# Kernel tuning notes

Measured on AMD Instinct MI355X. Metric: run time of the kernel, lower is better.

The kernel has to match this reference:

```python
import jax, jax.numpy as jnp
import numpy as np

N_BATCH = 8192   # rows/cols of score matrix
N_NEG = 16       # negatives per row (init kwarg n)
VOCAB = 100000   # item id range for sel_out


def setup_inputs() -> dict:
    key = jax.random.key(0)
    k1, k2 = jax.random.split(key)
    x = jax.random.normal(k1, (N_BATCH, N_BATCH), dtype=jnp.float32)
    sel_out = jax.random.randint(k2, (N_BATCH,), 0, VOCAB, dtype=jnp.int32)
    return {"x": x, "sel_out": sel_out}


def reference(x, sel_out):
    # mask[i, j] = 1 where item j differs from row i's target item
    mask = (sel_out[None, :] != sel_out[:, None]).astype(x.dtype)  # (n, n)
    # positive term: diagonal holds each row's target score
    pos = -jnp.mean(jax.nn.log_sigmoid(jnp.diagonal(x)))
    # top-N_NEG highest masked scores per row -> negative sample indices
    _, idx = jax.lax.top_k(x * mask, N_NEG)          # idx: (n, N_NEG)
    neg_vals = jnp.take_along_axis(x, idx, axis=1)   # gather raw scores
    # log(1 - sigmoid(v)) == log_sigmoid(-v) (numerically stable form)
    neg = -jnp.mean(jax.nn.log_sigmoid(-neg_vals))
    return pos + neg
```

## Files before the change

### kernel.cpp

```cpp
#include <hip/hip_runtime.h>
#include <math.h>

#define N_ROWS 8192
#define N_NEG 16
#define NBLK (N_ROWS / 8)

__device__ __forceinline__ float log_sigmoid(float v) {
    return fminf(v, 0.0f) - log1pf(__expf(-fabsf(v)));
}

#define INSERT(mv)                                                          \
    {                                                                       \
        unsigned long long ball = __ballot((mv) > tau);                     \
        while (ball) {                                                      \
            const int src = __ffsll((unsigned long long)ball) - 1;          \
            const float cand = __shfl((mv), src);                           \
            ball &= ball - 1;                                               \
            if (cand > tau) {                                               \
                float tprev = __shfl_up(t, 1);                              \
                if (lane == 0) tprev = 3.0e38f;                             \
                t = (t >= cand) ? t : (tprev >= cand ? cand : tprev);       \
                tau = __shfl(t, 15);                                        \
                ball &= __ballot((mv) > tau);         \
            }                                                               \
        }                                                                   \
    }

__global__ __launch_bounds__(512) void nsl_topk_kernel(
        const float* __restrict__ x,
        const int*   __restrict__ sel,
        float*       __restrict__ ws) {
    __shared__ int   sel_lds[N_ROWS];
    __shared__ float partial[8];

    {
        const int4* s4 = reinterpret_cast<const int4*>(sel);
        int4*       d4 = reinterpret_cast<int4*>(sel_lds);
#pragma unroll
        for (int k = 0; k < 4; ++k)
            d4[k * 512 + threadIdx.x] = s4[k * 512 + threadIdx.x];
    }
    __syncthreads();

    const int lane = threadIdx.x & 63;
    const int wid  = threadIdx.x >> 6;
    const int row  = (blockIdx.x << 3) + wid;

    const int    seli = sel_lds[row];
    const float* xrow = x + (size_t)row * N_ROWS;
    const float* pw   = xrow + lane * 4;

    float t   = -3.0e38f;
    float tau = -3.0e38f;

    float4 buf[4];
#pragma unroll
    for (int j = 0; j < 4; ++j)
        buf[j] = *reinterpret_cast<const float4*>(pw + j * 256);

#define BODY(c, PREFETCH)                                                   \
    {                                                                       \
        const float4 v = buf[(c) & 3];                                      \
        if (PREFETCH)                                                       \
            buf[(c) & 3] =                                                  \
                *reinterpret_cast<const float4*>(pw + ((c) + 4) * 256);     \
        const float mxv = fmaxf(fmaxf(v.x, v.y), fmaxf(v.z, v.w));          \
                       \
        if (__any(mxv > tau)) {                                             \
            const int4 s = *reinterpret_cast<const int4*>(                  \
                &sel_lds[((c) << 8) + (lane << 2)]);                        \
            const float m0 = (s.x != seli) ? v.x : 0.0f;                    \
            const float m1 = (s.y != seli) ? v.y : 0.0f;                    \
            const float m2 = (s.z != seli) ? v.z : 0.0f;                    \
            const float m3 = (s.w != seli) ? v.w : 0.0f;                    \
            INSERT(m0);                                                     \
            INSERT(m1);                                                     \
            INSERT(m2);                                                     \
            INSERT(m3);                                                     \
        }                                                                   \
    }

#pragma unroll 1
    for (int g = 0; g < 7; ++g) {
#pragma unroll
        for (int j = 0; j < 4; ++j) BODY((g << 2) + j, true);
    }
#pragma unroll
    for (int j = 0; j < 4; ++j) BODY(28 + j, false);
#undef BODY

    float ls = (lane < 16) ? log_sigmoid(-t) : 0.0f;
    ls += __shfl_xor(ls, 8);
    ls += __shfl_xor(ls, 4);
    ls += __shfl_xor(ls, 2);
    ls += __shfl_xor(ls, 1);

    if (lane == 0) {
        const float d = xrow[row];
        partial[wid] = -log_sigmoid(d) * (1.0f / (float)N_ROWS)
                       - ls * (1.0f / ((float)N_ROWS * (float)N_NEG));
    }
    __syncthreads();

    if (threadIdx.x == 0) {
        float s = 0.0f;
#pragma unroll
        for (int w = 0; w < 8; ++w) s += partial[w];
        ws[blockIdx.x] = s;
    }
}

__global__ __launch_bounds__(256) void nsl_reduce_kernel(
        const float* __restrict__ ws, float* __restrict__ out) {
    __shared__ float red[4];
    float s = 0.0f;
#pragma unroll
    for (int k = 0; k < NBLK / 256; ++k) s += ws[k * 256 + threadIdx.x];
    s += __shfl_xor(s, 32);
    s += __shfl_xor(s, 16);
    s += __shfl_xor(s, 8);
    s += __shfl_xor(s, 4);
    s += __shfl_xor(s, 2);
    s += __shfl_xor(s, 1);
    const int lane = threadIdx.x & 63, wid = threadIdx.x >> 6;
    if (lane == 0) red[wid] = s;
    __syncthreads();
    if (threadIdx.x == 0)
        out[0] = red[0] + red[1] + red[2] + red[3];
}

extern "C" void kernel_launch(void* const* d_in, const int* in_sizes, int n_in,
                              void* d_out, int out_size, void* d_ws, size_t ws_size,
                              hipStream_t stream) {
    const float* x   = (const float*)d_in[0];
    const int*   sel = (const int*)d_in[1];
    float* out = (float*)d_out;
    float* ws  = (float*)d_ws;

    nsl_topk_kernel<<<dim3(NBLK), dim3(512), 0, stream>>>(x, sel, ws);
    nsl_reduce_kernel<<<dim3(1), dim3(256), 0, stream>>>(ws, out);
}
```

Before: 65.04 us.

## Replace wave-serial top-k insertion with per-lane top-5 med3 networks plus exact fallback

Each lane now keeps its own sorted top-5 list, updated branch-free with fmax/fmed3 for every element. The 16 global maxima are then extracted by repeated wave-wide max reductions. If any lane's 5th value still exceeds the 16th global maximum, the lane may have dropped candidates, so the row is rescanned with the old serial ballot/shuffle insertion to stay exact. This removes the per-candidate ballot/shuffle serialization from the common path. In exchange every element costs about five ALU ops, and rows that hit the fallback are read a second time.

```diff
diff --git a/kernel.cpp b/kernel.cpp
--- a/kernel.cpp
+++ b/kernel.cpp
@@ -4,29 +4,34 @@
 #define N_ROWS 8192
 #define N_NEG 16
 #define NBLK (N_ROWS / 8)
+#define NEG_INF (-3.0e38f)
 
 __device__ __forceinline__ float log_sigmoid(float v) {
     return fminf(v, 0.0f) - log1pf(__expf(-fabsf(v)));
 }
 
-#define INSERT(mv)                                                          \
-    {                                                                       \
-        unsigned long long ball = __ballot((mv) > tau);                     \
-        while (ball) {                                                      \
-            const int src = __ffsll((unsigned long long)ball) - 1;          \
-            const float cand = __shfl((mv), src);                           \
-            ball &= ball - 1;                                               \
-            if (cand > tau) {                                               \
-                float tprev = __shfl_up(t, 1);                              \
-                if (lane == 0) tprev = 3.0e38f;                             \
-                t = (t >= cand) ? t : (tprev >= cand ? cand : tprev);       \
-                tau = __shfl(t, 15);                                        \
-                ball &= __ballot((mv) > tau);         \
-            }                                                               \
-        }                                                                   \
+__device__ __forceinline__ float wave_max64(float v) {
+    v = fmaxf(v, __shfl_xor(v, 1));
+    v = fmaxf(v, __shfl_xor(v, 2));
+    v = fmaxf(v, __shfl_xor(v, 4));
+    v = fmaxf(v, __shfl_xor(v, 8));
+    v = fmaxf(v, __shfl_xor(v, 16));
+    v = fmaxf(v, __shfl_xor(v, 32));
+    return v;
+}
+
+#define INS5(cexpr)                                                     \
+    {                                                                   \
+        const float _c = (cexpr);                                       \
+        const float n0 = fmaxf(t0, _c);                                 \
+        const float n1 = __builtin_amdgcn_fmed3f(_c, t0, t1);           \
+        const float n2 = __builtin_amdgcn_fmed3f(_c, t1, t2);           \
+        const float n3 = __builtin_amdgcn_fmed3f(_c, t2, t3);           \
+        const float n4 = __builtin_amdgcn_fmed3f(_c, t3, t4);           \
+        t0 = n0; t1 = n1; t2 = n2; t3 = n3; t4 = n4;                    \
     }
 
-__global__ __launch_bounds__(512) void nsl_topk_kernel(
+__global__ __launch_bounds__(512, 8) void nsl_topk_kernel(
         const float* __restrict__ x,
         const int*   __restrict__ sel,
         float*       __restrict__ ws) {
@@ -48,57 +53,95 @@
 
     const int    seli = sel_lds[row];
     const float* xrow = x + (size_t)row * N_ROWS;
-    const float* pw   = xrow + lane * 4;
+    const float* pw   = xrow + (lane << 2);
 
-    float t   = -3.0e38f;
-    float tau = -3.0e38f;
+    float t0 = NEG_INF, t1 = NEG_INF, t2 = NEG_INF, t3 = NEG_INF, t4 = NEG_INF;
 
-    float4 buf[4];
-#pragma unroll
-    for (int j = 0; j < 4; ++j)
-        buf[j] = *reinterpret_cast<const float4*>(pw + j * 256);
+#define LOADB(c) (*reinterpret_cast<const float4*>(pw + ((c) << 8)))
+#define CONSUME(c, bx, PF)                                              \
+    {                                                                   \
+        const float4 v = bx;                                            \
+        if (PF) bx = LOADB((c) + 4);                                    \
+        const int4 s = *reinterpret_cast<const int4*>(                  \
+            &sel_lds[((c) << 8) + (lane << 2)]);                        \
+        INS5((s.x != seli) ? v.x : 0.0f);                               \
+        INS5((s.y != seli) ? v.y : 0.0f);                               \
+        INS5((s.z != seli) ? v.z : 0.0f);                               \
+        INS5((s.w != seli) ? v.w : 0.0f);                               \
+    }
 
-#define BODY(c, PREFETCH)                                                   \
-    {                                                                       \
-        const float4 v = buf[(c) & 3];                                      \
-        if (PREFETCH)                                                       \
-            buf[(c) & 3] =                                                  \
-                *reinterpret_cast<const float4*>(pw + ((c) + 4) * 256);     \
-        const float mxv = fmaxf(fmaxf(v.x, v.y), fmaxf(v.z, v.w));          \
-                       \
-        if (__any(mxv > tau)) {                                             \
-            const int4 s = *reinterpret_cast<const int4*>(                  \
-                &sel_lds[((c) << 8) + (lane << 2)]);                        \
-            const float m0 = (s.x != seli) ? v.x : 0.0f;                    \
-            const float m1 = (s.y != seli) ? v.y : 0.0f;                    \
-            const float m2 = (s.z != seli) ? v.z : 0.0f;                    \
-            const float m3 = (s.w != seli) ? v.w : 0.0f;                    \
-            INSERT(m0);                                                     \
-            INSERT(m1);                                                     \
-            INSERT(m2);                                                     \
-            INSERT(m3);                                                     \
-        }                                                                   \
-    }
+    float4 b0 = LOADB(0), b1 = LOADB(1), b2 = LOADB(2), b3 = LOADB(3);
 
 #pragma unroll 1
     for (int g = 0; g < 7; ++g) {
+        const int c = g << 2;
+        CONSUME(c + 0, b0, true);
+        CONSUME(c + 1, b1, true);
+        CONSUME(c + 2, b2, true);
+        CONSUME(c + 3, b3, true);
+    }
+    CONSUME(28, b0, false);
+    CONSUME(29, b1, false);
+    CONSUME(30, b2, false);
+    CONSUME(31, b3, false);
+#undef CONSUME
+
+    const float t4_orig = t4;
+    float negsum = 0.0f;
+    float tau16  = 0.0f;
+#pragma unroll 1
+    for (int r = 0; r < 16; ++r) {
+        const float h = wave_max64(t0);
+        negsum += log_sigmoid(-h);
+        tau16 = h;
+        const unsigned long long b = __ballot(t0 == h);
+        if (lane == (__ffsll(b) - 1)) {
+            t0 = t1; t1 = t2; t2 = t3; t3 = t4; t4 = NEG_INF;
+        }
+    }
+
+    if (__any(t4_orig > tau16)) {
+        float dt = NEG_INF, tau = NEG_INF;
+#pragma unroll 1
+        for (int c = 0; c < 32; ++c) {
+            const float4 v = LOADB(c);
+            const int4 s = *reinterpret_cast<const int4*>(
+                &sel_lds[(c << 8) + (lane << 2)]);
+            float m[4];
+            m[0] = (s.x != seli) ? v.x : 0.0f;
+            m[1] = (s.y != seli) ? v.y : 0.0f;
+            m[2] = (s.z != seli) ? v.z : 0.0f;
+            m[3] = (s.w != seli) ? v.w : 0.0f;
 #pragma unroll
-        for (int j = 0; j < 4; ++j) BODY((g << 2) + j, true);
+            for (int k = 0; k < 4; ++k) {
+                unsigned long long ball = __ballot(m[k] > tau);
+                while (ball) {
+                    const int src = __ffsll(ball) - 1;
+                    const float cand = __shfl(m[k], src);
+                    ball &= ball - 1;
+                    if (cand > tau) {
+                        float tprev = __shfl_up(dt, 1);
+                        if (lane == 0) tprev = 3.0e38f;
+                        dt = (dt >= cand) ? dt : (tprev >= cand ? cand : tprev);
+                        tau = __shfl(dt, 15);
+                        ball &= __ballot(m[k] > tau);
+                    }
+                }
+            }
+        }
+        float ls = (lane < 16) ? log_sigmoid(-dt) : 0.0f;
+        ls += __shfl_xor(ls, 8);
+        ls += __shfl_xor(ls, 4);
+        ls += __shfl_xor(ls, 2);
+        ls += __shfl_xor(ls, 1);
+        negsum = ls;
     }
-#pragma unroll
-    for (int j = 0; j < 4; ++j) BODY(28 + j, false);
-#undef BODY
-
-    float ls = (lane < 16) ? log_sigmoid(-t) : 0.0f;
-    ls += __shfl_xor(ls, 8);
-    ls += __shfl_xor(ls, 4);
-    ls += __shfl_xor(ls, 2);
-    ls += __shfl_xor(ls, 1);
+#undef LOADB
 
     if (lane == 0) {
         const float d = xrow[row];
         partial[wid] = -log_sigmoid(d) * (1.0f / (float)N_ROWS)
-                       - ls * (1.0f / ((float)N_ROWS * (float)N_NEG));
+                       - negsum * (1.0f / ((float)N_ROWS * (float)N_NEG));
     }
     __syncthreads();
 
```

Result: slower. 84.97 us (+30.6%).
